# Kernel tuning notes

Measured on AMD Instinct MI355X. Metric: run time of the kernel, lower is better.

## Reference

```python
import jax, jax.numpy as jnp
import numpy as np

N_NODES = 100000
N_EDGES = 1600000
N_GRAPHS = 2048
BN_EPS = 1e-5


def _bn(h, gamma, beta):
    # BatchNorm1d in training mode: biased batch stats over the node axis
    mean = jnp.mean(h, axis=0)
    var = jnp.var(h, axis=0)
    return gamma * (h - mean) * jax.lax.rsqrt(var + BN_EPS) + beta


def _gin_layer(x, src, dst, w1, b1, gamma, beta, w2, b2):
    # GINConv with eps=0: mlp(x + sum_{j->i} x_j)
    agg = jax.ops.segment_sum(x[src], dst, num_segments=N_NODES)
    h = agg + x
    h = h @ w1 + b1
    h = jax.nn.relu(_bn(h, gamma, beta))
    h = h @ w2 + b2
    return jax.nn.relu(h)  # outer F.relu after GINConv (dropout = identity in eval)


def setup_inputs() -> dict:
    key = jax.random.key(0)
    ks = jax.random.split(key, 24)
    d = {}
    d['x'] = jax.random.normal(ks[0], (N_NODES, 66), dtype=jnp.float32)
    d['edge_index'] = jax.random.randint(ks[1], (2, N_EDGES), 0, N_NODES, dtype=jnp.int64)
    d['batch'] = jnp.sort(jax.random.randint(ks[2], (N_NODES,), 0, N_GRAPHS, dtype=jnp.int64))
    dims = [(66, 128), (128, 256), (256, 128)]
    ki = 3
    for li, (din, dout) in enumerate(dims):
        s1 = 1.0 / np.sqrt(din)
        s2 = 1.0 / np.sqrt(dout)
        d[f'g{li}_w1'] = jax.random.uniform(ks[ki + 0], (din, dout), jnp.float32, -s1, s1)
        d[f'g{li}_b1'] = jax.random.uniform(ks[ki + 1], (dout,), jnp.float32, -s1, s1)
        d[f'g{li}_gamma'] = jnp.ones((dout,), jnp.float32)
        d[f'g{li}_beta'] = jnp.zeros((dout,), jnp.float32)
        d[f'g{li}_w2'] = jax.random.uniform(ks[ki + 2], (dout, dout), jnp.float32, -s2, s2)
        d[f'g{li}_b2'] = jax.random.uniform(ks[ki + 3], (dout,), jnp.float32, -s2, s2)
        ki += 4
    fcd = [(128, 1024), (1024, 128)]
    for li, (din, dout) in enumerate(fcd):
        s = 1.0 / np.sqrt(din)
        d[f'fc{li}_w'] = jax.random.uniform(ks[ki + 0], (din, dout), jnp.float32, -s, s)
        d[f'fc{li}_b'] = jax.random.uniform(ks[ki + 1], (dout,), jnp.float32, -s, s)
        ki += 2
    return d


def reference(x, edge_index, batch,
              g0_w1, g0_b1, g0_gamma, g0_beta, g0_w2, g0_b2,
              g1_w1, g1_b1, g1_gamma, g1_beta, g1_w2, g1_b2,
              g2_w1, g2_b1, g2_gamma, g2_beta, g2_w2, g2_b2,
              fc0_w, fc0_b, fc1_w, fc1_b):
    src, dst = edge_index[0], edge_index[1]
    h = _gin_layer(x, src, dst, g0_w1, g0_b1, g0_gamma, g0_beta, g0_w2, g0_b2)
    h = _gin_layer(h, src, dst, g1_w1, g1_b1, g1_gamma, g1_beta, g1_w2, g1_b2)
    h = _gin_layer(h, src, dst, g2_w1, g2_b1, g2_gamma, g2_beta, g2_w2, g2_b2)
    # global_add_pool over graphs
    g = jax.ops.segment_sum(h, batch, num_segments=N_GRAPHS)
    g = jax.nn.relu(g @ fc0_w + fc0_b)
    return g @ fc1_w + fc1_b
```

## Files before the change

### kernel.cpp

```cpp
#include <hip/hip_runtime.h>

#define NNODES 100000
#define NEDGES 1600000
#define NGRAPHS 2048
#define BN_EPS 1e-5f

typedef __attribute__((ext_vector_type(8))) short bf16x8;
typedef __attribute__((ext_vector_type(4))) float f32x4;

__device__ __forceinline__ short f2bf(float x) {
    unsigned u = __float_as_uint(x);
    unsigned r = u + 0x7FFF + ((u >> 16) & 1);
    return (short)(r >> 16);
}
__device__ __forceinline__ float bf2f(short h) {
    return __uint_as_float(((unsigned)(unsigned short)h) << 16);
}

__global__ __launch_bounds__(256) void deg_kernel(const int* __restrict__ dstA,
                                                  int* __restrict__ deg) {
    int e = blockIdx.x * 256 + threadIdx.x;
    if (e < NEDGES) atomicAdd(&deg[dstA[e]], 1);
}

__global__ __launch_bounds__(256) void scan1_kernel(const int* __restrict__ deg,
                                                    int* __restrict__ partials) {
    int b = blockIdx.x;
    int i = b * 256 + threadIdx.x;
    int v = (i < NNODES) ? deg[i] : 0;
    __shared__ int wsum[4];
#pragma unroll
    for (int off = 32; off; off >>= 1) v += __shfl_down(v, off);
    if ((threadIdx.x & 63) == 0) wsum[threadIdx.x >> 6] = v;
    __syncthreads();
    if (threadIdx.x == 0) partials[b] = wsum[0] + wsum[1] + wsum[2] + wsum[3];
}

__global__ __launch_bounds__(512) void scan2_kernel(int* __restrict__ partials, int nb) {
    __shared__ int s[512];
    int t = threadIdx.x;
    int v = (t < nb) ? partials[t] : 0;
    s[t] = v;
    __syncthreads();
    for (int off = 1; off < 512; off <<= 1) {
        int u = (t >= off) ? s[t - off] : 0;
        __syncthreads();
        s[t] += u;
        __syncthreads();
    }
    if (t < nb) partials[t] = s[t] - v;
}

__global__ __launch_bounds__(256) void scan3_kernel(const int* __restrict__ deg,
                                                    const int* __restrict__ partials,
                                                    int* __restrict__ rowptr,
                                                    int* __restrict__ cursor,
                                                    const int* __restrict__ batch,
                                                    int* __restrict__ gstart) {
    int b = blockIdx.x;
    int t = threadIdx.x;
    int i = b * 256 + t;
    __shared__ int s[256];
    int v = (i < NNODES) ? deg[i] : 0;
    s[t] = v;
    __syncthreads();
    for (int off = 1; off < 256; off <<= 1) {
        int u = (t >= off) ? s[t - off] : 0;
        __syncthreads();
        s[t] += u;
        __syncthreads();
    }
    if (i < NNODES) {
        int ex = partials[b] + s[t] - v;
        rowptr[i] = ex;
        cursor[i] = ex;
        int bb = batch[i];
        int bp = (i == 0) ? -1 : batch[i - 1];
        for (int g = bp + 1; g <= bb; ++g) gstart[g] = i;
        if (i == NNODES - 1)
            for (int g = bb + 1; g <= NGRAPHS; ++g) gstart[g] = NNODES;
    }
    if (b == 0 && t == 0) rowptr[NNODES] = NEDGES;
}

__global__ __launch_bounds__(256) void fill_kernel(const int* __restrict__ srcA,
                                                   const int* __restrict__ dstA,
                                                   int* __restrict__ cursor,
                                                   int* __restrict__ adj) {
    int e = blockIdx.x * 256 + threadIdx.x;
    if (e < NEDGES) {
        int d = dstA[e];
        int loc = atomicAdd(&cursor[d], 1);
        adj[loc] = srcA[e];
    }
}

template <int DIM, int CHUNK, int OSTRIDE>
__global__ __launch_bounds__(256) void gather_kernel(const float* __restrict__ x,
                                                     const int* __restrict__ rowptr,
                                                     const int* __restrict__ adj,
                                                     float* __restrict__ agg,
                                                     const float* __restrict__ bias) {
    constexpr int PE = DIM / CHUNK;
    int gid = blockIdx.x * 256 + threadIdx.x;
    if (gid >= NNODES * PE) return;
    int node = gid / PE;
    int c = gid - node * PE;
    const int beg = rowptr[node];
    const int end = rowptr[node + 1];
    if (CHUNK == 4) {
        const float4* xp = (const float4*)x;
        float4 acc = xp[(size_t)node * PE + c];
        float4 acc1 = make_float4(0.f, 0.f, 0.f, 0.f);
        int i = beg;
        for (; i + 4 <= end; i += 4) {
            int s0 = adj[i + 0];
            int s1 = adj[i + 1];
            int s2 = adj[i + 2];
            int s3 = adj[i + 3];
            float4 v0 = xp[(size_t)s0 * PE + c];
            float4 v1 = xp[(size_t)s1 * PE + c];
            float4 v2 = xp[(size_t)s2 * PE + c];
            float4 v3 = xp[(size_t)s3 * PE + c];
            acc.x += v0.x + v1.x;
            acc.y += v0.y + v1.y;
            acc.z += v0.z + v1.z;
            acc.w += v0.w + v1.w;
            acc1.x += v2.x + v3.x;
            acc1.y += v2.y + v3.y;
            acc1.z += v2.z + v3.z;
            acc1.w += v2.w + v3.w;
        }
        for (; i < end; ++i) {
            int s = adj[i];
            float4 v = xp[(size_t)s * PE + c];
            acc.x += v.x;
            acc.y += v.y;
            acc.z += v.z;
            acc.w += v.w;
        }
        acc.x += acc1.x;
        acc.y += acc1.y;
        acc.z += acc1.z;
        acc.w += acc1.w;
        if (bias) {
            float4 b = *(const float4*)&bias[c * 4];
            acc.x += b.x; acc.y += b.y; acc.z += b.z; acc.w += b.w;
        }
        *(float4*)&agg[(size_t)node * OSTRIDE + c * 4] = acc;
    } else {
        const float2* xp = (const float2*)x;
        float2 acc = xp[(size_t)node * PE + c];
        float2 acc1 = make_float2(0.f, 0.f);
        int i = beg;
        for (; i + 4 <= end; i += 4) {
            int s0 = adj[i + 0];
            int s1 = adj[i + 1];
            int s2 = adj[i + 2];
            int s3 = adj[i + 3];
            float2 v0 = xp[(size_t)s0 * PE + c];
            float2 v1 = xp[(size_t)s1 * PE + c];
            float2 v2 = xp[(size_t)s2 * PE + c];
            float2 v3 = xp[(size_t)s3 * PE + c];
            acc.x += v0.x + v1.x;
            acc.y += v0.y + v1.y;
            acc1.x += v2.x + v3.x;
            acc1.y += v2.y + v3.y;
        }
        for (; i < end; ++i) {
            int s = adj[i];
            float2 v = xp[(size_t)s * PE + c];
            acc.x += v.x;
            acc.y += v.y;
        }
        acc.x += acc1.x;
        acc.y += acc1.y;
        *(float2*)&agg[(size_t)node * OSTRIDE + c * 2] = acc;
    }
}

template <int N>
__global__ __launch_bounds__(256) void bnstats_kernel(const float* __restrict__ h,
                                                      float* __restrict__ sums) {
    constexpr int SHIFT = (N == 128) ? 7 : 8;
    int t = blockIdx.x * 256 + threadIdx.x;
    int col = t & (N - 1);
    int slice = t >> SHIFT;
    float s = 0.f, s2 = 0.f;
    for (int r = slice; r < NNODES; r += 256) {
        float v = h[(size_t)r * N + col];
        s += v;
        s2 += v * v;
    }
    atomicAdd(&sums[col], s);
    atomicAdd(&sums[256 + col], s2);
}

__global__ void bnfinal_kernel(float* __restrict__ sums, const float* __restrict__ gamma,
                               const float* __restrict__ beta, float* __restrict__ scsh, int N,
                               float invM) {
    int c = threadIdx.x;
    if (c < N) {
        float mean = sums[c] * invM;
        float var = sums[256 + c] * invM - mean * mean;
        float sc = gamma[c] * rsqrtf(var + BN_EPS);
        scsh[c] = sc;
        scsh[256 + c] = beta[c] - mean * sc;
    }
    sums[c] = 0.f;
    sums[256 + c] = 0.f;
}

__global__ __launch_bounds__(256) void wprep_kernel(const float* __restrict__ W, int Kw, int N,
                                                    int KT, short* __restrict__ whi,
                                                    short* __restrict__ wlo) {
    int idx = blockIdx.x * 256 + threadIdx.x;
    int total = (N >> 4) * KT * 512;
    if (idx >= total) return;
    int j = idx & 7;
    int lane = (idx >> 3) & 63;
    int t = idx >> 9;
    int kt = t % KT;
    int nt = t / KT;
    int k = kt * 32 + ((lane >> 4) << 3) + j;
    int n = (nt << 4) + (lane & 15);
    float w = (k < Kw) ? W[(size_t)k * N + n] : 0.f;
    short hi = f2bf(w);
    short lo = f2bf(w - bf2f(hi));
    whi[idx] = hi;
    wlo[idx] = lo;
}

template <int NT, bool BNRELU_A, bool RELU_OUT, bool FUSE_STATS, bool SPLITK>
__global__ __launch_bounds__(256) void gemm_mfma_kernel(
    const float* __restrict__ A, const short* __restrict__ whi, const short* __restrict__ wlo,
    const float* __restrict__ bias, const float* __restrict__ scsh, float* __restrict__ C,
    float* __restrict__ stats, int M, int Kst, int KT, int N, int ktc) {
    __shared__ float sstat[512];
    const int tid = threadIdx.x;
    const int wave = tid >> 6;
    const int lane = tid & 63;
    const int quad = lane >> 4;
    const int l16 = lane & 15;
    const int mrow = blockIdx.x * 64 + wave * 16 + l16;
    const int ngrp = blockIdx.y * NT * 16;
    const size_t wgrp = (size_t)blockIdx.y * NT * KT * 512;
    const int ktbeg = SPLITK ? blockIdx.z * ktc : 0;
    const int ktend = SPLITK ? ktbeg + ktc : KT;
    float* Cb = SPLITK ? C + (size_t)blockIdx.z * M * N : C;

    if (FUSE_STATS) {
        sstat[tid] = 0.f;
        sstat[tid + 256] = 0.f;
        __syncthreads();
    }

    f32x4 acc[NT] = {};

    for (int kt = ktbeg; kt < ktend; ++kt) {
        const int kq = kt * 32 + quad * 8;
        const float* ap = A + (size_t)mrow * Kst + kq;
        float4 x0 = *(const float4*)ap;
        float4 x1 = *(const float4*)(ap + 4);
        float a8[8] = {x0.x, x0.y, x0.z, x0.w, x1.x, x1.y, x1.z, x1.w};
        if (BNRELU_A) {
            float4 sc0 = *(const float4*)&scsh[kq];
            float4 sc1 = *(const float4*)&scsh[kq + 4];
            float4 sh0 = *(const float4*)&scsh[256 + kq];
            float4 sh1 = *(const float4*)&scsh[256 + kq + 4];
            float sc[8] = {sc0.x, sc0.y, sc0.z, sc0.w, sc1.x, sc1.y, sc1.z, sc1.w};
            float sh[8] = {sh0.x, sh0.y, sh0.z, sh0.w, sh1.x, sh1.y, sh1.z, sh1.w};
#pragma unroll
            for (int i = 0; i < 8; ++i) a8[i] = fmaxf(a8[i] * sc[i] + sh[i], 0.f);
        }
        bf16x8 ahi, alo;
#pragma unroll
        for (int i = 0; i < 8; ++i) {
            short h = f2bf(a8[i]);
            ahi[i] = h;
            alo[i] = f2bf(a8[i] - bf2f(h));
        }
#pragma unroll
        for (int nt = 0; nt < NT; ++nt) {
            const size_t boff = wgrp + (((size_t)nt * KT + kt) << 9) + (lane << 3);
            bf16x8 bh = *(const bf16x8*)(whi + boff);
            bf16x8 bl = *(const bf16x8*)(wlo + boff);
            acc[nt] = __builtin_amdgcn_mfma_f32_16x16x32_bf16(ahi, bh, acc[nt], 0, 0, 0);
            acc[nt] = __builtin_amdgcn_mfma_f32_16x16x32_bf16(alo, bh, acc[nt], 0, 0, 0);
            acc[nt] = __builtin_amdgcn_mfma_f32_16x16x32_bf16(ahi, bl, acc[nt], 0, 0, 0);
            acc[nt] = __builtin_amdgcn_mfma_f32_16x16x32_bf16(alo, bl, acc[nt], 0, 0, 0);
        }
    }

    const int mbase = blockIdx.x * 64 + wave * 16 + quad * 4;
#pragma unroll
    for (int nt = 0; nt < NT; ++nt) {
        int gn = ngrp + nt * 16 + l16;
        float bv = bias ? bias[gn] : 0.f;
        float s = 0.f, s2 = 0.f;
#pragma unroll
        for (int r = 0; r < 4; ++r) {
            int gm = mbase + r;
            float v = acc[nt][r] + bv;
            if (RELU_OUT) v = fmaxf(v, 0.f);
            if (gm < M) {
                Cb[(size_t)gm * N + gn] = v;
                if (FUSE_STATS) {
                    s += v;
                    s2 += v * v;
                }
            }
        }
        if (FUSE_STATS) {
            s += __shfl_xor(s, 16);
            s += __shfl_xor(s, 32);
            s2 += __shfl_xor(s2, 16);
            s2 += __shfl_xor(s2, 32);
            if (quad == 0) {
                atomicAdd(&sstat[gn], s);
                atomicAdd(&sstat[256 + gn], s2);
            }
        }
    }
    if (FUSE_STATS) {
        __syncthreads();
        if (tid < N) {
            atomicAdd(&stats[tid], sstat[tid]);
            atomicAdd(&stats[256 + tid], sstat[256 + tid]);
        }
    }
}

__global__ __launch_bounds__(256) void splitk_reduce_kernel(const float* __restrict__ part,
                                                            const float* __restrict__ bias,
                                                            float* __restrict__ out) {
    const int i4 = blockIdx.x * 256 + threadIdx.x;
    const int TOT4 = NGRAPHS * 128 / 4;
    if (i4 >= TOT4) return;
    const float4* p = (const float4*)part;
    float4 acc = make_float4(0.f, 0.f, 0.f, 0.f);
#pragma unroll
    for (int c = 0; c < 8; ++c) {
        float4 v = p[(size_t)c * TOT4 + i4];
        acc.x += v.x; acc.y += v.y; acc.z += v.z; acc.w += v.w;
    }
    float4 b = ((const float4*)bias)[i4 & 31];
    acc.x += b.x; acc.y += b.y; acc.z += b.z; acc.w += b.w;
    ((float4*)out)[i4] = acc;
}

__global__ __launch_bounds__(128) void pool_seg_kernel(const float* __restrict__ h,
                                                       const int* __restrict__ gstart,
                                                       float* __restrict__ g) {
    int gr = blockIdx.x;
    int t = threadIdx.x;
    int beg = gstart[gr];
    int end = gstart[gr + 1];
    float acc = 0.f;
    for (int r = beg; r < end; ++r) acc += h[(size_t)r * 128 + t];
    g[(size_t)gr * 128 + t] = acc;
}

extern "C" void kernel_launch(void* const* d_in, const int* in_sizes, int n_in, void* d_out,
                              int out_size, void* d_ws, size_t ws_size, hipStream_t stream) {
    const float* x = (const float*)d_in[0];
    const int* ei = (const int*)d_in[1];
    const int* batch = (const int*)d_in[2];
    const int* srcA = ei;
    const int* dstA = ei + NEDGES;

    const float* g0_w1 = (const float*)d_in[3];
    const float* g0_b1 = (const float*)d_in[4];
    const float* g0_ga = (const float*)d_in[5];
    const float* g0_be = (const float*)d_in[6];
    const float* g0_w2 = (const float*)d_in[7];
    const float* g0_b2 = (const float*)d_in[8];
    const float* g1_w1 = (const float*)d_in[9];
    const float* g1_b1 = (const float*)d_in[10];
    const float* g1_ga = (const float*)d_in[11];
    const float* g1_be = (const float*)d_in[12];
    const float* g1_w2 = (const float*)d_in[13];
    const float* g1_b2 = (const float*)d_in[14];
    const float* g2_w1 = (const float*)d_in[15];
    const float* g2_b1 = (const float*)d_in[16];
    const float* g2_ga = (const float*)d_in[17];
    const float* g2_be = (const float*)d_in[18];
    const float* g2_w2 = (const float*)d_in[19];
    const float* g2_b2 = (const float*)d_in[20];
    const float* fc0_w = (const float*)d_in[21];
    const float* fc0_b = (const float*)d_in[22];
    const float* fc1_w = (const float*)d_in[23];
    const float* fc1_b = (const float*)d_in[24];

    float* ws = (float*)d_ws;
    const size_t BUF = (size_t)NNODES * 256;
    float* R0 = ws;
    float* R1 = R0 + BUF;
    float* stats = R1 + BUF;
    float* scsh = stats + 512;
    float* g = scsh + 512;
    float* gh = g + (size_t)NGRAPHS * 128;
    int* deg = (int*)(gh + (size_t)NGRAPHS * 1024);
    int* rowptr = deg + NNODES;
    int* cursor = rowptr + NNODES + 4;
    int* adj = cursor + NNODES;
    int* partials = adj + NEDGES;
    int* gstart = partials + 512;
    short* wf = (short*)(gstart + 2052);
    short* whi[8];
    short* wlo[8];
    for (int i = 0; i < 6; ++i) {
        whi[i] = wf + (size_t)i * 131072;
        wlo[i] = whi[i] + 65536;
    }
    whi[6] = wf + 6 * 131072;
    wlo[6] = whi[6] + 131072;
    whi[7] = whi[6] + 262144;
    wlo[7] = whi[7] + 131072;

    const int GB = (NNODES + 63) / 64;
    const int NB = (NNODES + 255) / 256;

    hipMemsetAsync(deg, 0, NNODES * sizeof(int), stream);
    hipMemsetAsync(stats, 0, 512 * sizeof(float), stream);
    deg_kernel<<<(NEDGES + 255) / 256, 256, 0, stream>>>(dstA, deg);
    scan1_kernel<<<NB, 256, 0, stream>>>(deg, partials);
    scan2_kernel<<<1, 512, 0, stream>>>(partials, NB);
    scan3_kernel<<<NB, 256, 0, stream>>>(deg, partials, rowptr, cursor, batch, gstart);
    fill_kernel<<<(NEDGES + 255) / 256, 256, 0, stream>>>(srcA, dstA, cursor, adj);

    wprep_kernel<<<(8 * 3 * 512 + 255) / 256, 256, 0, stream>>>(g0_w1, 66, 128, 3, whi[0], wlo[0]);
    wprep_kernel<<<(8 * 4 * 512 + 255) / 256, 256, 0, stream>>>(g0_w2, 128, 128, 4, whi[1], wlo[1]);
    wprep_kernel<<<(16 * 4 * 512 + 255) / 256, 256, 0, stream>>>(g1_w1, 128, 256, 4, whi[2], wlo[2]);
    wprep_kernel<<<(16 * 8 * 512 + 255) / 256, 256, 0, stream>>>(g1_w2, 256, 256, 8, whi[3], wlo[3]);
    wprep_kernel<<<(8 * 8 * 512 + 255) / 256, 256, 0, stream>>>(g2_w1, 256, 128, 8, whi[4], wlo[4]);
    wprep_kernel<<<(8 * 4 * 512 + 255) / 256, 256, 0, stream>>>(g2_w2, 128, 128, 4, whi[5], wlo[5]);
    wprep_kernel<<<(64 * 4 * 512 + 255) / 256, 256, 0, stream>>>(fc0_w, 128, 1024, 4, whi[6], wlo[6]);
    wprep_kernel<<<(8 * 32 * 512 + 255) / 256, 256, 0, stream>>>(fc1_w, 1024, 128, 32, whi[7], wlo[7]);

    gather_kernel<66, 2, 68><<<(NNODES * 33 + 255) / 256, 256, 0, stream>>>(x, rowptr, adj, R0,
                                                                            nullptr);
    gemm_mfma_kernel<8, false, false, true, false><<<GB, 256, 0, stream>>>(
        R0, whi[0], wlo[0], g0_b1, nullptr, R1, stats, NNODES, 68, 3, 128, 0);
    bnfinal_kernel<<<1, 256, 0, stream>>>(stats, g0_ga, g0_be, scsh, 128, 1.0f / NNODES);
    gemm_mfma_kernel<8, true, true, false, false><<<GB, 256, 0, stream>>>(
        R1, whi[1], wlo[1], g0_b2, scsh, R0, nullptr, NNODES, 128, 4, 128, 0);

    gather_kernel<128, 4, 128><<<(NNODES * 32 + 255) / 256, 256, 0, stream>>>(R0, rowptr, adj, R1,
                                                                              nullptr);
    gemm_mfma_kernel<16, false, false, true, false><<<GB, 256, 0, stream>>>(
        R1, whi[2], wlo[2], g1_b1, nullptr, R0, stats, NNODES, 128, 4, 256, 0);
    bnfinal_kernel<<<1, 256, 0, stream>>>(stats, g1_ga, g1_be, scsh, 256, 1.0f / NNODES);
    gemm_mfma_kernel<16, true, true, false, false><<<GB, 256, 0, stream>>>(
        R0, whi[3], wlo[3], g1_b2, scsh, R1, nullptr, NNODES, 256, 8, 256, 0);

    gemm_mfma_kernel<8, false, false, false, false><<<GB, 256, 0, stream>>>(
        R1, whi[4], wlo[4], nullptr, nullptr, R0, nullptr, NNODES, 256, 8, 128, 0);
    gather_kernel<128, 4, 128><<<(NNODES * 32 + 255) / 256, 256, 0, stream>>>(R0, rowptr, adj, R1,
                                                                              g2_b1);
    bnstats_kernel<128><<<128, 256, 0, stream>>>(R1, stats);
    bnfinal_kernel<<<1, 256, 0, stream>>>(stats, g2_ga, g2_be, scsh, 128, 1.0f / NNODES);
    gemm_mfma_kernel<8, true, true, false, false><<<GB, 256, 0, stream>>>(
        R1, whi[5], wlo[5], g2_b2, scsh, R0, nullptr, NNODES, 128, 4, 128, 0);

    pool_seg_kernel<<<NGRAPHS, 128, 0, stream>>>(R0, gstart, g);

    gemm_mfma_kernel<8, false, true, false, false><<<dim3(NGRAPHS / 64, 8), 256, 0, stream>>>(
        g, whi[6], wlo[6], fc0_b, nullptr, gh, nullptr, NGRAPHS, 128, 4, 1024, 0);
    gemm_mfma_kernel<8, false, false, false, true><<<dim3(NGRAPHS / 64, 1, 8), 256, 0, stream>>>(
        gh, whi[7], wlo[7], nullptr, nullptr, R1, nullptr, NGRAPHS, 1024, 32, 128, 4);
    splitk_reduce_kernel<<<(NGRAPHS * 128 / 4 + 255) / 256, 256, 0, stream>>>(R1, fc1_b,
                                                                              (float*)d_out);
}
```

Baseline: 1.213 ms.

## Store pre-split bf16 hi/lo activations from producers and add N-dimension grid split

Gather, pool and selected GEMM epilogues now write activations as separate bf16 hi/lo arrays, so downstream MFMA GEMMs load ready-split operands instead of converting fp32 in the inner loop. The 256-wide GEMMs switch from NT=16 to NT=8 with a 2-column grid, the K loop becomes a compile-time count, and launch bounds ask for 4 blocks per CU. This is meant to cut conversion ALU work and register pressure and to raise occupancy. The cost is extra buffer aliasing and zero-padding of the first-layer K to 96.

```diff
diff --git a/kernel.cpp b/kernel.cpp
--- a/kernel.cpp
+++ b/kernel.cpp
@@ -95,20 +95,40 @@
     }
 }
 
-template <int DIM, int CHUNK, int OSTRIDE>
+template <int DIM, int CHUNK, int OSTRIDE, bool SPLIT>
 __global__ __launch_bounds__(256) void gather_kernel(const float* __restrict__ x,
                                                      const int* __restrict__ rowptr,
                                                      const int* __restrict__ adj,
                                                      float* __restrict__ agg,
+                                                     short* __restrict__ oh,
+                                                     short* __restrict__ ol,
                                                      const float* __restrict__ bias) {
     constexpr int PE = DIM / CHUNK;
+    constexpr int PEL = SPLIT ? (OSTRIDE / CHUNK) : PE;
     int gid = blockIdx.x * 256 + threadIdx.x;
-    if (gid >= NNODES * PE) return;
-    int node = gid / PE;
-    int c = gid - node * PE;
+    if (gid >= NNODES * PEL) return;
+    int node = gid / PEL;
+    int c = gid - node * PEL;
+    if constexpr (SPLIT) {
+        if (c >= PE) {
+            size_t o = (size_t)node * OSTRIDE + c * CHUNK;
+            if constexpr (CHUNK == 4) {
+                short4 z;
+                z.x = z.y = z.z = z.w = 0;
+                *(short4*)&oh[o] = z;
+                *(short4*)&ol[o] = z;
+            } else {
+                short2 z;
+                z.x = z.y = 0;
+                *(short2*)&oh[o] = z;
+                *(short2*)&ol[o] = z;
+            }
+            return;
+        }
+    }
     const int beg = rowptr[node];
     const int end = rowptr[node + 1];
-    if (CHUNK == 4) {
+    if constexpr (CHUNK == 4) {
         const float4* xp = (const float4*)x;
         float4 acc = xp[(size_t)node * PE + c];
         float4 acc1 = make_float4(0.f, 0.f, 0.f, 0.f);
@@ -145,9 +165,27 @@
         acc.w += acc1.w;
         if (bias) {
             float4 b = *(const float4*)&bias[c * 4];
-            acc.x += b.x; acc.y += b.y; acc.z += b.z; acc.w += b.w;
-        }
-        *(float4*)&agg[(size_t)node * OSTRIDE + c * 4] = acc;
+            acc.x += b.x;
+            acc.y += b.y;
+            acc.z += b.z;
+            acc.w += b.w;
+        }
+        if constexpr (SPLIT) {
+            size_t o = (size_t)node * OSTRIDE + c * 4;
+            short4 h4, l4;
+            h4.x = f2bf(acc.x);
+            l4.x = f2bf(acc.x - bf2f(h4.x));
+            h4.y = f2bf(acc.y);
+            l4.y = f2bf(acc.y - bf2f(h4.y));
+            h4.z = f2bf(acc.z);
+            l4.z = f2bf(acc.z - bf2f(h4.z));
+            h4.w = f2bf(acc.w);
+            l4.w = f2bf(acc.w - bf2f(h4.w));
+            *(short4*)&oh[o] = h4;
+            *(short4*)&ol[o] = l4;
+        } else {
+            *(float4*)&agg[(size_t)node * OSTRIDE + c * 4] = acc;
+        }
     } else {
         const float2* xp = (const float2*)x;
         float2 acc = xp[(size_t)node * PE + c];
@@ -175,7 +213,18 @@
         }
         acc.x += acc1.x;
         acc.y += acc1.y;
-        *(float2*)&agg[(size_t)node * OSTRIDE + c * 2] = acc;
+        if constexpr (SPLIT) {
+            size_t o = (size_t)node * OSTRIDE + c * 2;
+            short2 h2, l2;
+            h2.x = f2bf(acc.x);
+            l2.x = f2bf(acc.x - bf2f(h2.x));
+            h2.y = f2bf(acc.y);
+            l2.y = f2bf(acc.y - bf2f(h2.y));
+            *(short2*)&oh[o] = h2;
+            *(short2*)&ol[o] = l2;
+        } else {
+            *(float2*)&agg[(size_t)node * OSTRIDE + c * 2] = acc;
+        }
     }
 }
 
@@ -231,11 +280,13 @@
     wlo[idx] = lo;
 }
 
-template <int NT, bool BNRELU_A, bool RELU_OUT, bool FUSE_STATS, bool SPLITK>
-__global__ __launch_bounds__(256) void gemm_mfma_kernel(
-    const float* __restrict__ A, const short* __restrict__ whi, const short* __restrict__ wlo,
-    const float* __restrict__ bias, const float* __restrict__ scsh, float* __restrict__ C,
-    float* __restrict__ stats, int M, int Kst, int KT, int N, int ktc) {
+template <int NT, int KTLOOP, bool BNRELU_A, bool RELU_OUT, bool FUSE_STATS, bool SPLITK,
+          bool ASPLIT, bool SPLIT_OUT>
+__global__ __launch_bounds__(256, 4) void gemm_mfma_kernel(
+    const float* __restrict__ A, const short* __restrict__ Ah, const short* __restrict__ Al,
+    const short* __restrict__ whi, const short* __restrict__ wlo, const float* __restrict__ bias,
+    const float* __restrict__ scsh, float* __restrict__ C, short* __restrict__ Ch,
+    short* __restrict__ Cl, float* __restrict__ stats, int M, int Kst, int KT, int N) {
     __shared__ float sstat[512];
     const int tid = threadIdx.x;
     const int wave = tid >> 6;
@@ -245,8 +296,7 @@
     const int mrow = blockIdx.x * 64 + wave * 16 + l16;
     const int ngrp = blockIdx.y * NT * 16;
     const size_t wgrp = (size_t)blockIdx.y * NT * KT * 512;
-    const int ktbeg = SPLITK ? blockIdx.z * ktc : 0;
-    const int ktend = SPLITK ? ktbeg + ktc : KT;
+    const int ktbeg = SPLITK ? blockIdx.z * KTLOOP : 0;
     float* Cb = SPLITK ? C + (size_t)blockIdx.z * M * N : C;
 
     if (FUSE_STATS) {
@@ -257,32 +307,37 @@
 
     f32x4 acc[NT] = {};
 
-    for (int kt = ktbeg; kt < ktend; ++kt) {
+    auto kstep = [&](int kt) {
         const int kq = kt * 32 + quad * 8;
-        const float* ap = A + (size_t)mrow * Kst + kq;
-        float4 x0 = *(const float4*)ap;
-        float4 x1 = *(const float4*)(ap + 4);
-        float a8[8] = {x0.x, x0.y, x0.z, x0.w, x1.x, x1.y, x1.z, x1.w};
-        if (BNRELU_A) {
-            float4 sc0 = *(const float4*)&scsh[kq];
-            float4 sc1 = *(const float4*)&scsh[kq + 4];
-            float4 sh0 = *(const float4*)&scsh[256 + kq];
-            float4 sh1 = *(const float4*)&scsh[256 + kq + 4];
-            float sc[8] = {sc0.x, sc0.y, sc0.z, sc0.w, sc1.x, sc1.y, sc1.z, sc1.w};
-            float sh[8] = {sh0.x, sh0.y, sh0.z, sh0.w, sh1.x, sh1.y, sh1.z, sh1.w};
-#pragma unroll
-            for (int i = 0; i < 8; ++i) a8[i] = fmaxf(a8[i] * sc[i] + sh[i], 0.f);
-        }
         bf16x8 ahi, alo;
-#pragma unroll
-        for (int i = 0; i < 8; ++i) {
-            short h = f2bf(a8[i]);
-            ahi[i] = h;
-            alo[i] = f2bf(a8[i] - bf2f(h));
+        if constexpr (ASPLIT) {
+            ahi = *(const bf16x8*)(Ah + (size_t)mrow * Kst + kq);
+            alo = *(const bf16x8*)(Al + (size_t)mrow * Kst + kq);
+        } else {
+            const float* ap = A + (size_t)mrow * Kst + kq;
+            float4 x0 = *(const float4*)ap;
+            float4 x1 = *(const float4*)(ap + 4);
+            float a8[8] = {x0.x, x0.y, x0.z, x0.w, x1.x, x1.y, x1.z, x1.w};
+            if constexpr (BNRELU_A) {
+                float4 sc0 = *(const float4*)&scsh[kq];
+                float4 sc1 = *(const float4*)&scsh[kq + 4];
+                float4 sh0 = *(const float4*)&scsh[256 + kq];
+                float4 sh1 = *(const float4*)&scsh[256 + kq + 4];
+                float sc[8] = {sc0.x, sc0.y, sc0.z, sc0.w, sc1.x, sc1.y, sc1.z, sc1.w};
+                float sh[8] = {sh0.x, sh0.y, sh0.z, sh0.w, sh1.x, sh1.y, sh1.z, sh1.w};
+#pragma unroll
+                for (int i = 0; i < 8; ++i) a8[i] = fmaxf(a8[i] * sc[i] + sh[i], 0.f);
+            }
+#pragma unroll
+            for (int i = 0; i < 8; ++i) {
+                short h = f2bf(a8[i]);
+                ahi[i] = h;
+                alo[i] = f2bf(a8[i] - bf2f(h));
+            }
         }
 #pragma unroll
         for (int nt = 0; nt < NT; ++nt) {
-            const size_t boff = wgrp + (((size_t)nt * KT + kt) << 9) + (lane << 3);
+            const size_t boff = wgrp + (((size_t)nt * KT + kt) << 9) + ((size_t)lane << 3);
             bf16x8 bh = *(const bf16x8*)(whi + boff);
             bf16x8 bl = *(const bf16x8*)(wlo + boff);
             acc[nt] = __builtin_amdgcn_mfma_f32_16x16x32_bf16(ahi, bh, acc[nt], 0, 0, 0);
@@ -290,6 +345,14 @@
             acc[nt] = __builtin_amdgcn_mfma_f32_16x16x32_bf16(ahi, bl, acc[nt], 0, 0, 0);
             acc[nt] = __builtin_amdgcn_mfma_f32_16x16x32_bf16(alo, bl, acc[nt], 0, 0, 0);
         }
+    };
+
+    if constexpr (ASPLIT) {
+#pragma unroll 2
+        for (int k = 0; k < KTLOOP; ++k) kstep(ktbeg + k);
+    } else {
+#pragma unroll 1
+        for (int k = 0; k < KTLOOP; ++k) kstep(ktbeg + k);
     }
 
     const int mbase = blockIdx.x * 64 + wave * 16 + quad * 4;
@@ -304,7 +367,13 @@
             float v = acc[nt][r] + bv;
             if (RELU_OUT) v = fmaxf(v, 0.f);
             if (gm < M) {
-                Cb[(size_t)gm * N + gn] = v;
+                if constexpr (SPLIT_OUT) {
+                    short h = f2bf(v);
+                    Ch[(size_t)gm * N + gn] = h;
+                    Cl[(size_t)gm * N + gn] = f2bf(v - bf2f(h));
+                } else {
+                    Cb[(size_t)gm * N + gn] = v;
+                }
                 if (FUSE_STATS) {
                     s += v;
                     s2 += v * v;
@@ -342,23 +411,38 @@
 #pragma unroll
     for (int c = 0; c < 8; ++c) {
         float4 v = p[(size_t)c * TOT4 + i4];
-        acc.x += v.x; acc.y += v.y; acc.z += v.z; acc.w += v.w;
+        acc.x += v.x;
+        acc.y += v.y;
+        acc.z += v.z;
+        acc.w += v.w;
     }
     float4 b = ((const float4*)bias)[i4 & 31];
-    acc.x += b.x; acc.y += b.y; acc.z += b.z; acc.w += b.w;
+    acc.x += b.x;
+    acc.y += b.y;
+    acc.z += b.z;
+    acc.w += b.w;
     ((float4*)out)[i4] = acc;
 }
 
+template <bool SPLIT>
 __global__ __launch_bounds__(128) void pool_seg_kernel(const float* __restrict__ h,
                                                        const int* __restrict__ gstart,
-                                                       float* __restrict__ g) {
+                                                       float* __restrict__ g,
+                                                       short* __restrict__ oh,
+                                                       short* __restrict__ ol) {
     int gr = blockIdx.x;
     int t = threadIdx.x;
     int beg = gstart[gr];
     int end = gstart[gr + 1];
     float acc = 0.f;
     for (int r = beg; r < end; ++r) acc += h[(size_t)r * 128 + t];
-    g[(size_t)gr * 128 + t] = acc;
+    if constexpr (SPLIT) {
+        short hh = f2bf(acc);
+        oh[(size_t)gr * 128 + t] = hh;
+        ol[(size_t)gr * 128 + t] = f2bf(acc - bf2f(hh));
+    } else {
+        g[(size_t)gr * 128 + t] = acc;
+    }
 }
 
 extern "C" void kernel_launch(void* const* d_in, const int* in_sizes, int n_in, void* d_out,
@@ -418,6 +502,17 @@
     whi[7] = whi[6] + 262144;
     wlo[7] = whi[7] + 131072;
 
+    short* P0h = (short*)R0;
+    short* P0l = P0h + (size_t)NNODES * 96;
+    short* P1h = (short*)R1;
+    short* P1l = P1h + (size_t)NNODES * 128;
+    short* P2h = (short*)R1;
+    short* P2l = P2h + (size_t)NNODES * 256;
+    short* GPh = (short*)g;
+    short* GPl = GPh + (size_t)NGRAPHS * 128;
+    short* GHh = (short*)gh;
+    short* GHl = GHh + (size_t)NGRAPHS * 1024;
+
     const int GB = (NNODES + 63) / 64;
     const int NB = (NNODES + 255) / 256;
 
@@ -435,40 +530,52 @@
     wprep_kernel<<<(16 * 8 * 512 + 255) / 256, 256, 0, stream>>>(g1_w2, 256, 256, 8, whi[3], wlo[3]);
     wprep_kernel<<<(8 * 8 * 512 + 255) / 256, 256, 0, stream>>>(g2_w1, 256, 128, 8, whi[4], wlo[4]);
     wprep_kernel<<<(8 * 4 * 512 + 255) / 256, 256, 0, stream>>>(g2_w2, 128, 128, 4, whi[5], wlo[5]);
-    wprep_kernel<<<(64 * 4 * 512 + 255) / 256, 256, 0, stream>>>(fc0_w, 128, 1024, 4, whi[6], wlo[6]);
-    wprep_kernel<<<(8 * 32 * 512 + 255) / 256, 256, 0, stream>>>(fc1_w, 1024, 128, 32, whi[7], wlo[7]);
-
-    gather_kernel<66, 2, 68><<<(NNODES * 33 + 255) / 256, 256, 0, stream>>>(x, rowptr, adj, R0,
-                                                                            nullptr);
-    gemm_mfma_kernel<8, false, false, true, false><<<GB, 256, 0, stream>>>(
-        R0, whi[0], wlo[0], g0_b1, nullptr, R1, stats, NNODES, 68, 3, 128, 0);
+    wprep_kernel<<<(64 * 4 * 512 + 255) / 256, 256, 0, stream>>>(fc0_w, 128, 1024, 4, whi[6],
+                                                                 wlo[6]);
+    wprep_kernel<<<(8 * 32 * 512 + 255) / 256, 256, 0, stream>>>(fc1_w, 1024, 128, 32, whi[7],
+                                                                 wlo[7]);
+
+    gather_kernel<66, 2, 96, true><<<(NNODES * 48 + 255) / 256, 256, 0, stream>>>(
+        x, rowptr, adj, nullptr, P0h, P0l, nullptr);
+    gemm_mfma_kernel<8, 3, false, false, true, false, true, false><<<GB, 256, 0, stream>>>(
+        nullptr, P0h, P0l, whi[0], wlo[0], g0_b1, nullptr, R1, nullptr, nullptr, stats, NNODES, 96,
+        3, 128);
     bnfinal_kernel<<<1, 256, 0, stream>>>(stats, g0_ga, g0_be, scsh, 128, 1.0f / NNODES);
-    gemm_mfma_kernel<8, true, true, false, false><<<GB, 256, 0, stream>>>(
-        R1, whi[1], wlo[1], g0_b2, scsh, R0, nullptr, NNODES, 128, 4, 128, 0);
-
-    gather_kernel<128, 4, 128><<<(NNODES * 32 + 255) / 256, 256, 0, stream>>>(R0, rowptr, adj, R1,
-                                                                              nullptr);
-    gemm_mfma_kernel<16, false, false, true, false><<<GB, 256, 0, stream>>>(
-        R1, whi[2], wlo[2], g1_b1, nullptr, R0, stats, NNODES, 128, 4, 256, 0);
+    gemm_mfma_kernel<8, 4, true, true, false, false, false, false><<<GB, 256, 0, stream>>>(
+        R1, nullptr, nullptr, whi[1], wlo[1], g0_b2, scsh, R0, nullptr, nullptr, nullptr, NNODES,
+        128, 4, 128);
+
+    gather_kernel<128, 4, 128, true><<<(NNODES * 32 + 255) / 256, 256, 0, stream>>>(
+        R0, rowptr, adj, nullptr, P1h, P1l, nullptr);
+    gemm_mfma_kernel<8, 4, false, false, true, false, true, false>
+        <<<dim3(GB, 2), 256, 0, stream>>>(nullptr, P1h, P1l, whi[2], wlo[2], g1_b1, nullptr, R0,
+                                          nullptr, nullptr, stats, NNODES, 128, 4, 256);
     bnfinal_kernel<<<1, 256, 0, stream>>>(stats, g1_ga, g1_be, scsh, 256, 1.0f / NNODES);
-    gemm_mfma_kernel<16, true, true, false, false><<<GB, 256, 0, stream>>>(
-        R0, whi[3], wlo[3], g1_b2, scsh, R1, nullptr, NNODES, 256, 8, 256, 0);
-
-    gemm_mfma_kernel<8, false, false, false, false><<<GB, 256, 0, stream>>>(
-        R1, whi[4], wlo[4], nullptr, nullptr, R0, nullptr, NNODES, 256, 8, 128, 0);
-    gather_kernel<128, 4, 128><<<(NNODES * 32 + 255) / 256, 256, 0, stream>>>(R0, rowptr, adj, R1,
-                                                                              g2_b1);
+    gemm_mfma_kernel<8, 8, true, true, false, false, false, true>
+        <<<dim3(GB, 2), 256, 0, stream>>>(R0, nullptr, nullptr, whi[3], wlo[3], g1_b2, scsh,
+                                          nullptr, P2h, P2l, nullptr, NNODES, 256, 8, 256);
+
+    gemm_mfma_kernel<8, 8, false, false, false, false, true, false><<<GB, 256, 0, stream>>>(
+        nullptr, P2h, P2l, whi[4], wlo[4], nullptr, nullptr, R0, nullptr, nullptr, nullptr, NNODES,
+        256, 8, 128);
+    gather_kernel<128, 4, 128, false><<<(NNODES * 32 + 255) / 256, 256, 0, stream>>>(
+        R0, rowptr, adj, R1, nullptr, nullptr, g2_b1);
     bnstats_kernel<128><<<128, 256, 0, stream>>>(R1, stats);
     bnfinal_kernel<<<1, 256, 0, stream>>>(stats, g2_ga, g2_be, scsh, 128, 1.0f / NNODES);
-    gemm_mfma_kernel<8, true, true, false, false><<<GB, 256, 0, stream>>>(
-        R1, whi[5], wlo[5], g2_b2, scsh, R0, nullptr, NNODES, 128, 4, 128, 0);
-
-    pool_seg_kernel<<<NGRAPHS, 128, 0, stream>>>(R0, gstart, g);
-
-    gemm_mfma_kernel<8, false, true, false, false><<<dim3(NGRAPHS / 64, 8), 256, 0, stream>>>(
-        g, whi[6], wlo[6], fc0_b, nullptr, gh, nullptr, NGRAPHS, 128, 4, 1024, 0);
-    gemm_mfma_kernel<8, false, false, false, true><<<dim3(NGRAPHS / 64, 1, 8), 256, 0, stream>>>(
-        gh, whi[7], wlo[7], nullptr, nullptr, R1, nullptr, NGRAPHS, 1024, 32, 128, 4);
+    gemm_mfma_kernel<8, 4, true, true, false, false, false, false><<<GB, 256, 0, stream>>>(
+        R1, nullptr, nullptr, whi[5], wlo[5], g2_b2, scsh, R0, nullptr, nullptr, nullptr, NNODES,
+        128, 4, 128);
+
+    pool_seg_kernel<true><<<NGRAPHS, 128, 0, stream>>>(R0, gstart, nullptr, GPh, GPl);
+
+    gemm_mfma_kernel<8, 4, false, true, false, false, true, true>
+        <<<dim3(NGRAPHS / 64, 8), 256, 0, stream>>>(nullptr, GPh, GPl, whi[6], wlo[6], fc0_b,
+                                                    nullptr, nullptr, GHh, GHl, nullptr, NGRAPHS,
+                                                    128, 4, 1024);
+    gemm_mfma_kernel<8, 4, false, false, false, true, true, false>
+        <<<dim3(NGRAPHS / 64, 1, 8), 256, 0, stream>>>(nullptr, GHh, GHl, whi[7], wlo[7], nullptr,
+                                                       nullptr, R1, nullptr, nullptr, nullptr,
+                                                       NGRAPHS, 1024, 32, 128);
     splitk_reduce_kernel<<<(NGRAPHS * 128 / 4 + 255) / 256, 256, 0, stream>>>(R1, fc1_b,
                                                                               (float*)d_out);
 }
```

Result: slower. 1.243 ms (+2.5%).
